# Kernel tuning notes

Hardware: AMD Instinct MI355X
Metric: run time of the kernel (lower is better)

## Reference

```python
import jax, jax.numpy as jnp
import numpy as np


def setup_inputs() -> dict:
    key = jax.random.key(0)
    ks = jax.random.split(key, 8)
    B, L, C = 8, 4096, 1024
    H = C // 2
    return {
        "x": jax.random.normal(ks[0], (B, L, C), dtype=jnp.float32),
        "w1": jax.random.normal(ks[1], (C, 1), dtype=jnp.float32) * 0.02,
        "b1": jnp.zeros((1,), dtype=jnp.float32),
        "w2": jax.random.normal(ks[2], (C, H), dtype=jnp.float32) * 0.02,
        "b2": jnp.zeros((H,), dtype=jnp.float32),
        "w3": jax.random.normal(ks[3], (H, C), dtype=jnp.float32) * 0.02,
        "b3": jnp.zeros((C,), dtype=jnp.float32),
        "w4": jax.random.normal(ks[4], (C, H), dtype=jnp.float32) * 0.02,
        "b4": jnp.zeros((H,), dtype=jnp.float32),
        "w5": jax.random.normal(ks[5], (C, H), dtype=jnp.float32) * 0.02,
        "b5": jnp.zeros((H,), dtype=jnp.float32),
    }


def reference(x, w1, b1, w2, b2, w3, b3, w4, b4, w5, b5):
    # Polarized self-attention (keras): channel branch then spatial branch.
    B, L, C = x.shape
    # --- channel branch ---
    t1 = x @ w1 + b1                                   # conv1: [B, L, 1]
    t2 = x @ w2 + b2                                   # conv2: [B, L, C/2]
    a = jax.nn.softmax(t1.reshape(B, 1, L), axis=-1)   # reshape1 + softmax: [B, 1, L]
    t2 = jnp.einsum('bol,blh->boh', a, t2)             # dot1 (axes 2,1): [B, 1, C/2]
    t2 = jax.nn.sigmoid(t2 @ w3 + b3)                  # conv3 + sigmoid: [B, 1, C]
    # attention1([inputs, t2]): dot scores [B, L, 1]; softmax over key axis of
    # size 1 is exactly 1.0, so output is t2 broadcast across L (exact math).
    o = jnp.broadcast_to(t2, (B, L, C))                # [B, L, C]
    # --- spatial branch ---
    t1 = o @ w4 + b4                                   # conv4: [B, L, C/2]
    t2 = o @ w5 + b5                                   # conv5: [B, L, C/2]
    t1 = jnp.max(t1, axis=1)[:, :, None]               # global max pool + reshape2: [B, C/2, 1]
    s = jax.nn.sigmoid(jnp.einsum('bho,blh->bol', t1, t2))  # dot2 (axes 1,2) + sigmoid: [B, 1, L]
    # attention2([reshape(o, [B,C,L]), s]): scores [B, C, 1]; softmax over the
    # size-1 key axis is 1.0, so output is s broadcast to [B, C, L] (exact).
    out = jnp.broadcast_to(s, (B, C, L)).reshape(B, L, C)  # reshape4
    return out
```

## Files before the change

### kernel.cpp

```cpp
#include <hip/hip_runtime.h>
#include <stdint.h>

#define B 8
#define L 4096
#define C 1024
#define H 512
#define NPART 512
#define CCH 16

__global__ __launch_bounds__(256) void kA_fused(const float* __restrict__ x,
                                                const float* __restrict__ w1,
                                                const float* __restrict__ b1,
                                                float* __restrict__ partial_xa,
                                                float* __restrict__ partial_s,
                                                float* __restrict__ zero_targets) {
    __shared__ float4 lds[4][256];
    __shared__ float ldsS[4];
    int t = threadIdx.x;
    int wave = t >> 6, lane = t & 63;
    int b = blockIdx.x >> 6;
    int blkInB = blockIdx.x & 63;
    int l0 = blkInB * 64 + wave * 16;
    float b1v = b1[0];

    if (blockIdx.x < 48) zero_targets[blockIdx.x * 256 + t] = 0.f;

    const float4* w1v = (const float4*)w1;
    float4 wf[4];
#pragma unroll
    for (int k = 0; k < 4; ++k) wf[k] = w1v[lane + 64 * k];

    float4 acc[4];
#pragma unroll
    for (int k = 0; k < 4; ++k) acc[k] = make_float4(0.f, 0.f, 0.f, 0.f);
    float sexp = 0.f;

    for (int r = 0; r < 16; ++r) {
        const float4* row = (const float4*)(x + ((size_t)(b * L + l0 + r)) * C);
        float4 xv[4];
#pragma unroll
        for (int k = 0; k < 4; ++k) xv[k] = row[lane + 64 * k];
        float d = 0.f;
#pragma unroll
        for (int k = 0; k < 4; ++k)
            d += xv[k].x * wf[k].x + xv[k].y * wf[k].y + xv[k].z * wf[k].z + xv[k].w * wf[k].w;
#pragma unroll
        for (int off = 32; off > 0; off >>= 1) d += __shfl_xor(d, off, 64);
        float e = __expf(d + b1v);
        sexp += e;
#pragma unroll
        for (int k = 0; k < 4; ++k) {
            acc[k].x += e * xv[k].x;
            acc[k].y += e * xv[k].y;
            acc[k].z += e * xv[k].z;
            acc[k].w += e * xv[k].w;
        }
    }
#pragma unroll
    for (int k = 0; k < 4; ++k) lds[wave][lane + 64 * k] = acc[k];
    if (lane == 0) ldsS[wave] = sexp;
    __syncthreads();
    float4 s0 = lds[0][t], s1 = lds[1][t], s2 = lds[2][t], s3 = lds[3][t];
    float4 s4;
    s4.x = (s0.x + s1.x) + (s2.x + s3.x);
    s4.y = (s0.y + s1.y) + (s2.y + s3.y);
    s4.z = (s0.z + s1.z) + (s2.z + s3.z);
    s4.w = (s0.w + s1.w) + (s2.w + s3.w);
    ((float4*)partial_xa)[(size_t)blockIdx.x * 256 + t] = s4;
    if (t == 0) partial_s[blockIdx.x] = (ldsS[0] + ldsS[1]) + (ldsS[2] + ldsS[3]);
}

__global__ __launch_bounds__(256) void k4a_pooled(const float* __restrict__ partial_xa,
                                                  const float* __restrict__ partial_s,
                                                  const float* __restrict__ w2,
                                                  const float* __restrict__ b2,
                                                  float* __restrict__ pooled) {
    __shared__ float ldsS[512];
    __shared__ float invS[B];
    __shared__ float xs[B][CCH];
    int hg = blockIdx.x & 1;
    int cc = blockIdx.x >> 1;
    int c0 = cc * CCH;
    int t = threadIdx.x;

    ldsS[t] = partial_s[t];
    ldsS[t + 256] = partial_s[t + 256];
    __syncthreads();
    if (t < B) {
        float s = 0.f;
        for (int i = 0; i < 64; ++i) s += ldsS[t * 64 + i];
        invS[t] = 1.f / s;
    }
    __syncthreads();

    if (t < B * CCH) {
        int bb = t >> 4, ci = t & 15;
        float s = 0.f;
        const float* src = partial_xa + (size_t)(bb * 64) * C + c0 + ci;
        for (int j = 0; j < 64; ++j) s += src[(size_t)j * C];
        xs[bb][ci] = s * invS[bb];
    }
    __syncthreads();

    int h = hg * 256 + t;
    float acc[B] = {0.f, 0.f, 0.f, 0.f, 0.f, 0.f, 0.f, 0.f};
#pragma unroll
    for (int ci = 0; ci < CCH; ++ci) {
        float w = w2[(size_t)(c0 + ci) * H + h];
#pragma unroll
        for (int bb = 0; bb < B; ++bb) acc[bb] += xs[bb][ci] * w;
    }
    float bias = (cc == 0) ? b2[h] : 0.f;
#pragma unroll
    for (int bb = 0; bb < B; ++bb) atomicAdd(&pooled[bb * H + h], acc[bb] + bias);
}

__global__ __launch_bounds__(256) void k4bc(const float* __restrict__ pooled,
                                            const float* __restrict__ w3,
                                            const float* __restrict__ b3,
                                            const float* __restrict__ w4,
                                            const float* __restrict__ w5,
                                            float* __restrict__ u4raw,
                                            float* __restrict__ u5raw) {
    __shared__ float pooledS[B][H];
    __shared__ float vpart[16][B][CCH];
    __shared__ float vs[B][CCH];
    int hg = blockIdx.x & 1;
    int cc = blockIdx.x >> 1;
    int c0 = cc * CCH;
    int t = threadIdx.x;

    for (int i = t; i < B * H; i += 256) ((float*)pooledS)[i] = pooled[i];
    __syncthreads();

    {
        int ci = t & 15;
        int hq = t >> 4;
        float a[B] = {0.f, 0.f, 0.f, 0.f, 0.f, 0.f, 0.f, 0.f};
        for (int hh = 0; hh < 32; ++hh) {
            int h = hq * 32 + hh;
            float w = w3[(size_t)h * C + c0 + ci];
#pragma unroll
            for (int bb = 0; bb < B; ++bb) a[bb] += pooledS[bb][h] * w;
        }
#pragma unroll
        for (int bb = 0; bb < B; ++bb) vpart[hq][bb][ci] = a[bb];
    }
    __syncthreads();
    if (t < B * CCH) {
        int bb = t >> 4, ci = t & 15;
        float v = b3[c0 + ci];
#pragma unroll
        for (int q = 0; q < 16; ++q) v += vpart[q][bb][ci];
        vs[bb][ci] = 1.f / (1.f + __expf(-v));
    }
    __syncthreads();
    {
        int h = hg * 256 + t;
        float a4[B] = {0.f, 0.f, 0.f, 0.f, 0.f, 0.f, 0.f, 0.f};
        float a5[B] = {0.f, 0.f, 0.f, 0.f, 0.f, 0.f, 0.f, 0.f};
#pragma unroll
        for (int ci = 0; ci < CCH; ++ci) {
            float wa = w4[(size_t)(c0 + ci) * H + h];
            float wb = w5[(size_t)(c0 + ci) * H + h];
#pragma unroll
            for (int bb = 0; bb < B; ++bb) {
                a4[bb] += vs[bb][ci] * wa;
                a5[bb] += vs[bb][ci] * wb;
            }
        }
#pragma unroll
        for (int bb = 0; bb < B; ++bb) {
            atomicAdd(&u4raw[bb * H + h], a4[bb]);
            atomicAdd(&u5raw[bb * H + h], a5[bb]);
        }
    }
}

__global__ __launch_bounds__(256) void k5_fill(const float* __restrict__ u4raw, const float* __restrict__ b4,
                                               const float* __restrict__ u5raw, const float* __restrict__ b5,
                                               float* __restrict__ out) {
    __shared__ float red[256];
    int blk = blockIdx.x, t = threadIdx.x;
    int b = blk >> 8;
    int rg = blk & 255;
    float s = (u4raw[b * H + t] + b4[t]) * (u5raw[b * H + t] + b5[t])
            + (u4raw[b * H + 256 + t] + b4[256 + t]) * (u5raw[b * H + 256 + t] + b5[256 + t]);
    red[t] = s; __syncthreads();
    for (int st = 128; st > 0; st >>= 1) { if (t < st) red[t] += red[t + st]; __syncthreads(); }
    float sc = 1.f / (1.f + __expf(-red[0]));
    float4 s4 = make_float4(sc, sc, sc, sc);
    float4* o = (float4*)out + (size_t)b * (L * C / 4) + (size_t)rg * 4096;
#pragma unroll
    for (int k = 0; k < 16; ++k) o[t + 256 * k] = s4;
}

extern "C" void kernel_launch(void* const* d_in, const int* in_sizes, int n_in,
                              void* d_out, int out_size, void* d_ws, size_t ws_size,
                              hipStream_t stream) {
    const float* x  = (const float*)d_in[0];
    const float* w1 = (const float*)d_in[1];
    const float* b1 = (const float*)d_in[2];
    const float* w2 = (const float*)d_in[3];
    const float* b2 = (const float*)d_in[4];
    const float* w3 = (const float*)d_in[5];
    const float* b3 = (const float*)d_in[6];
    const float* w4 = (const float*)d_in[7];
    const float* b4 = (const float*)d_in[8];
    const float* w5 = (const float*)d_in[9];
    const float* b5 = (const float*)d_in[10];

    float* ws         = (float*)d_ws;
    float* partial_xa = ws;
    float* partial_s  = partial_xa + NPART * C;
    float* pooled     = partial_s + NPART;
    float* u4raw      = pooled + B * H;
    float* u5raw      = u4raw + B * H;

    kA_fused<<<NPART, 256, 0, stream>>>(x, w1, b1, partial_xa, partial_s, pooled);
    k4a_pooled<<<128, 256, 0, stream>>>(partial_xa, partial_s, w2, b2, pooled);
    k4bc<<<128, 256, 0, stream>>>(pooled, w3, b3, w4, w5, u4raw, u5raw);
    k5_fill<<<2048, 256, 0, stream>>>(u4raw, b4, u5raw, b5, (float*)d_out);
}
```

Before: 281.7 us.

## Merge MLP kernels via grid-wide atomic barrier and precompute per-batch scalars

Fuses the pooled-projection kernel and the w3/w4/w5 kernel into one launch of 128 blocks. The blocks synchronise through a spin-wait on a global atomic counter. Block 0 then waits on a second counter and computes the 8 per-batch sigmoid scalars, so the fill kernel no longer repeats the 512-element dot-product reduction in each of its 2048 blocks. This removes one kernel launch and redundant reduction work. In exchange it adds spin barriers, which only work because all 128 blocks can be resident at once, and a serial tail in block 0.

```diff
diff --git a/kernel.cpp b/kernel.cpp
--- a/kernel.cpp
+++ b/kernel.cpp
@@ -7,6 +7,7 @@
 #define H 512
 #define NPART 512
 #define CCH 16
+#define NMLP 128
 
 __global__ __launch_bounds__(256) void kA_fused(const float* __restrict__ x,
                                                 const float* __restrict__ w1,
@@ -23,7 +24,7 @@
     int l0 = blkInB * 64 + wave * 16;
     float b1v = b1[0];
 
-    if (blockIdx.x < 48) zero_targets[blockIdx.x * 256 + t] = 0.f;
+    if (blockIdx.x < 50) zero_targets[blockIdx.x * 256 + t] = 0.f;
 
     const float4* w1v = (const float4*)w1;
     float4 wf[4];
@@ -70,14 +71,24 @@
     if (t == 0) partial_s[blockIdx.x] = (ldsS[0] + ldsS[1]) + (ldsS[2] + ldsS[3]);
 }
 
-__global__ __launch_bounds__(256) void k4a_pooled(const float* __restrict__ partial_xa,
-                                                  const float* __restrict__ partial_s,
-                                                  const float* __restrict__ w2,
-                                                  const float* __restrict__ b2,
-                                                  float* __restrict__ pooled) {
+__global__ __launch_bounds__(256) void k4_mlp(const float* __restrict__ partial_xa,
+                                              const float* __restrict__ partial_s,
+                                              const float* __restrict__ w2, const float* __restrict__ b2,
+                                              const float* __restrict__ w3, const float* __restrict__ b3,
+                                              const float* __restrict__ w4, const float* __restrict__ b4,
+                                              const float* __restrict__ w5, const float* __restrict__ b5,
+                                              float* __restrict__ pooled,
+                                              float* __restrict__ u4raw,
+                                              float* __restrict__ u5raw,
+                                              float* __restrict__ scal,
+                                              int* __restrict__ cnt) {
     __shared__ float ldsS[512];
     __shared__ float invS[B];
     __shared__ float xs[B][CCH];
+    __shared__ float pooledS[B][H];
+    __shared__ float vpart[16][B][CCH];
+    __shared__ float vs[B][CCH];
+    __shared__ float red[256];
     int hg = blockIdx.x & 1;
     int cc = blockIdx.x >> 1;
     int c0 = cc * CCH;
@@ -92,7 +103,6 @@
         invS[t] = 1.f / s;
     }
     __syncthreads();
-
     if (t < B * CCH) {
         int bb = t >> 4, ci = t & 15;
         float s = 0.f;
@@ -101,38 +111,30 @@
         xs[bb][ci] = s * invS[bb];
     }
     __syncthreads();
-
-    int h = hg * 256 + t;
-    float acc[B] = {0.f, 0.f, 0.f, 0.f, 0.f, 0.f, 0.f, 0.f};
-#pragma unroll
-    for (int ci = 0; ci < CCH; ++ci) {
-        float w = w2[(size_t)(c0 + ci) * H + h];
-#pragma unroll
-        for (int bb = 0; bb < B; ++bb) acc[bb] += xs[bb][ci] * w;
-    }
-    float bias = (cc == 0) ? b2[h] : 0.f;
-#pragma unroll
-    for (int bb = 0; bb < B; ++bb) atomicAdd(&pooled[bb * H + h], acc[bb] + bias);
-}
-
-__global__ __launch_bounds__(256) void k4bc(const float* __restrict__ pooled,
-                                            const float* __restrict__ w3,
-                                            const float* __restrict__ b3,
-                                            const float* __restrict__ w4,
-                                            const float* __restrict__ w5,
-                                            float* __restrict__ u4raw,
-                                            float* __restrict__ u5raw) {
-    __shared__ float pooledS[B][H];
-    __shared__ float vpart[16][B][CCH];
-    __shared__ float vs[B][CCH];
-    int hg = blockIdx.x & 1;
-    int cc = blockIdx.x >> 1;
-    int c0 = cc * CCH;
-    int t = threadIdx.x;
-
-    for (int i = t; i < B * H; i += 256) ((float*)pooledS)[i] = pooled[i];
-    __syncthreads();
-
+    {
+        int h = hg * 256 + t;
+        float acc[B] = {0.f, 0.f, 0.f, 0.f, 0.f, 0.f, 0.f, 0.f};
+#pragma unroll
+        for (int ci = 0; ci < CCH; ++ci) {
+            float w = w2[(size_t)(c0 + ci) * H + h];
+#pragma unroll
+            for (int bb = 0; bb < B; ++bb) acc[bb] += xs[bb][ci] * w;
+        }
+        float bias = (cc == 0) ? b2[h] : 0.f;
+#pragma unroll
+        for (int bb = 0; bb < B; ++bb) atomicAdd(&pooled[bb * H + h], acc[bb] + bias);
+    }
+    __syncthreads();
+    if (t == 0) {
+        __threadfence();
+        __hip_atomic_fetch_add(&cnt[0], 1, __ATOMIC_RELEASE, __HIP_MEMORY_SCOPE_AGENT);
+        while (__hip_atomic_load(&cnt[0], __ATOMIC_ACQUIRE, __HIP_MEMORY_SCOPE_AGENT) < NMLP) {}
+    }
+    __syncthreads();
+
+    for (int i = t; i < B * H; i += 256)
+        ((float*)pooledS)[i] = __hip_atomic_load(&pooled[i], __ATOMIC_RELAXED, __HIP_MEMORY_SCOPE_AGENT);
+    __syncthreads();
     {
         int ci = t & 15;
         int hq = t >> 4;
@@ -175,20 +177,42 @@
             atomicAdd(&u5raw[bb * H + h], a5[bb]);
         }
     }
-}
-
-__global__ __launch_bounds__(256) void k5_fill(const float* __restrict__ u4raw, const float* __restrict__ b4,
-                                               const float* __restrict__ u5raw, const float* __restrict__ b5,
+    __syncthreads();
+    if (blockIdx.x != 0) {
+        if (t == 0) {
+            __threadfence();
+            __hip_atomic_fetch_add(&cnt[1], 1, __ATOMIC_RELEASE, __HIP_MEMORY_SCOPE_AGENT);
+        }
+        return;
+    }
+    if (t == 0) {
+        __threadfence();
+        __hip_atomic_fetch_add(&cnt[1], 1, __ATOMIC_RELEASE, __HIP_MEMORY_SCOPE_AGENT);
+        while (__hip_atomic_load(&cnt[1], __ATOMIC_ACQUIRE, __HIP_MEMORY_SCOPE_AGENT) < NMLP) {}
+    }
+    __syncthreads();
+    for (int bb = 0; bb < B; ++bb) {
+        float s = 0.f;
+#pragma unroll
+        for (int p = 0; p < 2; ++p) {
+            int h = t + p * 256;
+            float a = __hip_atomic_load(&u4raw[bb * H + h], __ATOMIC_RELAXED, __HIP_MEMORY_SCOPE_AGENT) + b4[h];
+            float c = __hip_atomic_load(&u5raw[bb * H + h], __ATOMIC_RELAXED, __HIP_MEMORY_SCOPE_AGENT) + b5[h];
+            s += a * c;
+        }
+        red[t] = s; __syncthreads();
+        for (int st = 128; st > 0; st >>= 1) { if (t < st) red[t] += red[t + st]; __syncthreads(); }
+        if (t == 0) scal[bb] = 1.f / (1.f + __expf(-red[0]));
+        __syncthreads();
+    }
+}
+
+__global__ __launch_bounds__(256) void k5_fill(const float* __restrict__ scal,
                                                float* __restrict__ out) {
-    __shared__ float red[256];
     int blk = blockIdx.x, t = threadIdx.x;
     int b = blk >> 8;
     int rg = blk & 255;
-    float s = (u4raw[b * H + t] + b4[t]) * (u5raw[b * H + t] + b5[t])
-            + (u4raw[b * H + 256 + t] + b4[256 + t]) * (u5raw[b * H + 256 + t] + b5[256 + t]);
-    red[t] = s; __syncthreads();
-    for (int st = 128; st > 0; st >>= 1) { if (t < st) red[t] += red[t + st]; __syncthreads(); }
-    float sc = 1.f / (1.f + __expf(-red[0]));
+    float sc = scal[b];
     float4 s4 = make_float4(sc, sc, sc, sc);
     float4* o = (float4*)out + (size_t)b * (L * C / 4) + (size_t)rg * 4096;
 #pragma unroll
@@ -216,9 +240,11 @@
     float* pooled     = partial_s + NPART;
     float* u4raw      = pooled + B * H;
     float* u5raw      = u4raw + B * H;
+    float* scal       = u5raw + B * H;
+    int*   cnt        = (int*)(scal + 8);
 
     kA_fused<<<NPART, 256, 0, stream>>>(x, w1, b1, partial_xa, partial_s, pooled);
-    k4a_pooled<<<128, 256, 0, stream>>>(partial_xa, partial_s, w2, b2, pooled);
-    k4bc<<<128, 256, 0, stream>>>(pooled, w3, b3, w4, w5, u4raw, u5raw);
-    k5_fill<<<2048, 256, 0, stream>>>(u4raw, b4, u5raw, b5, (float*)d_out);
-}
+    k4_mlp<<<NMLP, 256, 0, stream>>>(partial_xa, partial_s, w2, b2, w3, b3,
+                                     w4, b4, w5, b5, pooled, u4raw, u5raw, scal, cnt);
+    k5_fill<<<2048, 256, 0, stream>>>(scal, (float*)d_out);
+}
```

Result: slower. 292.4 us (+3.8%).
